# Optimization experiments

Measured on AMD Instinct MI355X. Metric: run time of the kernel, lower is better.

The kernel has to match this reference:

```python
import jax, jax.numpy as jnp
import numpy as np

B, T, F = 512, 256, 24
CF = 64            # cnn_filters
IN = 2 * CF        # LNN input size after second conv
UNITS = 128        # lnn_units
DENSE = 64         # dense_units
ODE_UNFOLDS = 6    # semi-implicit ODE solver unfolds (LiquidNet default)


def _maxpool1d(x):  # [B,C,T] -> [B,C,T//2]
    return jax.lax.reduce_window(x, -jnp.inf, jax.lax.max, (1, 1, 2), (1, 1, 2), 'VALID')


def setup_inputs() -> dict:
    key = jax.random.key(0)
    ks = jax.random.split(key, 16)
    u = lambda k, shape, lo, hi: jax.random.uniform(k, shape, jnp.float32, lo, hi)
    return {
        'x': jax.random.normal(ks[0], (B, T, F), jnp.float32),
        'conv1_w': jax.random.normal(ks[1], (CF, F, 5), jnp.float32) * 0.1,
        'conv1_b': jnp.zeros((CF,), jnp.float32),
        'conv2_w': jax.random.normal(ks[2], (2 * CF, CF, 3), jnp.float32) * 0.1,
        'conv2_b': jnp.zeros((2 * CF,), jnp.float32),
        'input_w': jnp.ones((IN,), jnp.float32),
        'input_b': jnp.zeros((IN,), jnp.float32),
        'sensory_mu': u(ks[3], (IN, UNITS), 0.3, 0.8),
        'sensory_sigma': u(ks[4], (IN, UNITS), 3.0, 8.0),
        'sensory_W': u(ks[5], (IN, UNITS), 0.01, 1.0),
        'sensory_erev': jnp.sign(jax.random.normal(ks[6], (IN, UNITS))).astype(jnp.float32),
        'mu': u(ks[7], (UNITS, UNITS), 0.3, 0.8),
        'sigma': u(ks[8], (UNITS, UNITS), 3.0, 8.0),
        'W': u(ks[9], (UNITS, UNITS), 0.01, 1.0),
        'erev': jnp.sign(jax.random.normal(ks[10], (UNITS, UNITS))).astype(jnp.float32),
        'vleak': u(ks[11], (UNITS,), -0.2, 0.2),
        'gleak': jnp.ones((UNITS,), jnp.float32),
        'cm_t': jnp.full((UNITS,), 0.5, jnp.float32),
        'fc1_w': jax.random.normal(ks[12], (DENSE, UNITS), jnp.float32) * 0.05,
        'fc1_b': jnp.zeros((DENSE,), jnp.float32),
        'fc2_w': jax.random.normal(ks[13], (1, DENSE), jnp.float32) * 0.05,
        'fc2_b': jnp.zeros((1,), jnp.float32),
    }


def _forward(x, conv1_w, conv1_b, conv2_w, conv2_b, input_w, input_b,
             sensory_mu, sensory_sigma, sensory_W, sensory_erev,
             mu, sigma, W, erev, vleak, gleak, cm_t,
             fc1_w, fc1_b, fc2_w, fc2_b):
    # --- CNN feature extractor ---
    h = jnp.transpose(x, (0, 2, 1))                        # [B, F, T]
    dn = ('NCH', 'OIH', 'NCH')
    h = jax.lax.conv_general_dilated(h, conv1_w, (1,), 'SAME', dimension_numbers=dn)
    h = _maxpool1d(jax.nn.relu(h + conv1_b[None, :, None]))
    h = jax.lax.conv_general_dilated(h, conv2_w, (1,), 'SAME', dimension_numbers=dn)
    h = _maxpool1d(jax.nn.relu(h + conv2_b[None, :, None]))  # dropout: eval mode (identity)
    feats = jnp.transpose(h, (0, 2, 1))                    # [B, T/4, IN]
    xs = jnp.transpose(feats, (1, 0, 2))                   # [T', B, IN] for scan

    # --- LiquidNet (LTC) recurrence, semi-implicit ODE solver ---
    def step(v, xt):
        xt = xt * input_w + input_b                        # affine input mapping
        s_act = sensory_W * jax.nn.sigmoid((xt[:, :, None] - sensory_mu) * sensory_sigma)  # [B,IN,U]
        w_num_s = jnp.sum(s_act * sensory_erev, axis=1)    # [B,U]
        w_den_s = jnp.sum(s_act, axis=1)
        for _ in range(ODE_UNFOLDS):
            w_act = W * jax.nn.sigmoid((v[:, :, None] - mu) * sigma)  # [B,U,U]
            w_num = jnp.sum(w_act * erev, axis=1) + w_num_s
            w_den = jnp.sum(w_act, axis=1) + w_den_s
            v = (cm_t * v + gleak * vleak + w_num) / (cm_t + gleak + w_den)
        return v, None

    h0 = jnp.zeros((x.shape[0], UNITS), x.dtype)
    hT, _ = jax.lax.scan(jax.checkpoint(step), h0, xs)

    # --- MLP head ---
    y = jax.nn.relu(hT @ fc1_w.T + fc1_b)
    return y @ fc2_w.T + fc2_b                             # [B, 1]


def reference(x, conv1_w, conv1_b, conv2_w, conv2_b, input_w, input_b,
              sensory_mu, sensory_sigma, sensory_W, sensory_erev,
              mu, sigma, W, erev, vleak, gleak, cm_t,
              fc1_w, fc1_b, fc2_w, fc2_b):
    return _forward(x, conv1_w, conv1_b, conv2_w, conv2_b, input_w, input_b,
                    sensory_mu, sensory_sigma, sensory_W, sensory_erev,
                    mu, sigma, W, erev, vleak, gleak, cm_t,
                    fc1_w, fc1_b, fc2_w, fc2_b)
```

## Files before the change

kernel.cpp:

```cpp
#include <hip/hip_runtime.h>
#include <hip/hip_bf16.h>


#define L2E 1.4426950408889634f

__global__ __launch_bounds__(256)
void prep_kernel(const float* __restrict__ smu, const float* __restrict__ ssig,
                 const float* __restrict__ sW,  const float* __restrict__ serev,
                 const float* __restrict__ mu,  const float* __restrict__ sig,
                 const float* __restrict__ W,   const float* __restrict__ erev,
                 const float* __restrict__ in_w, const float* __restrict__ in_b,
                 float2* __restrict__ R12, float* __restrict__ VT,
                 float4* __restrict__ S4) {
  int idx = blockIdx.x * 256 + threadIdx.x;
  int i = idx >> 7;
  float r1 = sig[idx] * L2E;
  R12[idx] = make_float2(r1, mu[idx] * r1);
  VT[idx]  = W[idx] * erev[idx];
  float ss = ssig[idx] * L2E;
  S4[idx] = make_float4(ss * in_w[i], (smu[idx] - in_b[i]) * ss,
                        sW[idx] * serev[idx], 0.f);
}

__launch_bounds__(512)
__global__ void conv1_kernel(const float* __restrict__ x, const float* __restrict__ w1,
                             const float* __restrict__ b1, float* __restrict__ P1) {
  __shared__ float xs[6240];
  int tid = threadIdx.x, b = blockIdx.x;
  const float* xb = x + (size_t)b * 6144;
  for (int idx = tid; idx < 6144; idx += 512) xs[idx + 48] = xb[idx];
  if (tid < 48) { xs[tid] = 0.f; xs[6192 + tid] = 0.f; }
  __syncthreads();
  int tp = tid & 127, cq = tid >> 7;
  float acc0[16], acc1[16];
#pragma unroll
  for (int n = 0; n < 16; n++) { float bb = b1[cq * 16 + n]; acc0[n] = bb; acc1[n] = bb; }
  for (int cic = 0; cic < 3; cic++) {
    float p[6][8];
#pragma unroll
    for (int r = 0; r < 6; r++) {
      const float* row = &xs[(2 * tp + r) * 24 + cic * 8];
      float4 a = *(const float4*)row;
      float4 c = *(const float4*)(row + 4);
      p[r][0] = a.x; p[r][1] = a.y; p[r][2] = a.z; p[r][3] = a.w;
      p[r][4] = c.x; p[r][5] = c.y; p[r][6] = c.z; p[r][7] = c.w;
    }
#pragma unroll
    for (int n = 0; n < 16; n++) {
      const float* wr = w1 + (cq * 16 + n) * 120 + cic * 40;
#pragma unroll
      for (int c = 0; c < 8; c++) {
#pragma unroll
        for (int kk = 0; kk < 5; kk++) {
          float w = wr[c * 5 + kk];
          acc0[n] = fmaf(p[kk][c],     w, acc0[n]);
          acc1[n] = fmaf(p[kk + 1][c], w, acc1[n]);
        }
      }
    }
  }
  float* pb = P1 + (size_t)b * 8192;
#pragma unroll
  for (int n = 0; n < 16; n++)
    pb[(cq * 16 + n) * 128 + tp] = fmaxf(fmaxf(acc0[n], acc1[n]), 0.f);
}

__launch_bounds__(512)
__global__ void conv2_kernel(const float* __restrict__ P1, const float* __restrict__ w2,
                             const float* __restrict__ b2, float* __restrict__ feats) {
  __shared__ float xs[8450];
  int tid = threadIdx.x, b = blockIdx.x;
  const float* pb = P1 + (size_t)b * 8192;
  for (int idx = tid; idx < 8192; idx += 512) {
    int ci = idx >> 7, t = idx & 127;
    xs[(t + 1) * 65 + ci] = pb[idx];
  }
  if (tid < 65) { xs[tid] = 0.f; xs[129 * 65 + tid] = 0.f; }
  __syncthreads();
  int tp = tid & 63, cq = tid >> 6;
  float acc0[16], acc1[16];
#pragma unroll
  for (int n = 0; n < 16; n++) { float bb = b2[cq * 16 + n]; acc0[n] = bb; acc1[n] = bb; }
  for (int cic = 0; cic < 8; cic++) {
    float p[4][8];
#pragma unroll
    for (int r = 0; r < 4; r++)
#pragma unroll
      for (int c = 0; c < 8; c++)
        p[r][c] = xs[(2 * tp + r) * 65 + cic * 8 + c];
#pragma unroll
    for (int n = 0; n < 16; n++) {
      const float* wr = w2 + (cq * 16 + n) * 192 + cic * 24;
#pragma unroll
      for (int c = 0; c < 8; c++) {
#pragma unroll
        for (int kk = 0; kk < 3; kk++) {
          float w = wr[c * 3 + kk];
          acc0[n] = fmaf(p[kk][c],     w, acc0[n]);
          acc1[n] = fmaf(p[kk + 1][c], w, acc1[n]);
        }
      }
    }
  }
  __syncthreads();
#pragma unroll
  for (int n = 0; n < 16; n += 4) {
    float4 v;
    v.x = fmaxf(fmaxf(acc0[n],     acc1[n]),     0.f);
    v.y = fmaxf(fmaxf(acc0[n + 1], acc1[n + 1]), 0.f);
    v.z = fmaxf(fmaxf(acc0[n + 2], acc1[n + 2]), 0.f);
    v.w = fmaxf(fmaxf(acc0[n + 3], acc1[n + 3]), 0.f);
    *(float4*)&xs[tp * 128 + cq * 16 + n] = v;
  }
  __syncthreads();
  float* fb = feats + (size_t)b * 8192;
  for (int idx = tid; idx < 8192; idx += 512) fb[idx] = xs[idx];
}

__launch_bounds__(1024)
__global__ void lnn_kernel(const float2* __restrict__ R12, const float* __restrict__ VT,
                           const float4* __restrict__ S4,
                           const float* __restrict__ feats,
                           const float* __restrict__ cm_t, const float* __restrict__ gleak,
                           const float* __restrict__ vleak,
                           const float* __restrict__ fc1_w, const float* __restrict__ fc1_b,
                           const float* __restrict__ fc2_w, const float* __restrict__ fc2_b,
                           float* __restrict__ out) {
  __shared__ float2 r12lds[16384];
  __shared__ float4 psum[8][128];
  __shared__ float2 vs2[128];
  __shared__ float2 xt2[128];
  __shared__ float red[2][64];
  int tid = threadIdx.x;
  int j = tid & 127, h = tid >> 7;
  int b0 = blockIdx.x * 2;

  for (int idx = tid; idx < 16384; idx += 1024) r12lds[idx] = R12[idx];

  float vw[16];
#pragma unroll
  for (int n = 0; n < 16; n++) vw[n] = VT[(16 * h + n) * 128 + j];

  float cmj = cm_t[j], glk = gleak[j];
  float gvl = glk * vleak[j], cgl = cmj + glk;
  float vj0 = 0.f, vj1 = 0.f;
  if (tid < 128) vs2[j] = make_float2(0.f, 0.f);
  __syncthreads();

  for (int t = 0; t < 64; t++) {
    if (tid < 128) {
      float a = feats[(size_t)b0 * 8192 + t * 128 + j];
      float b = feats[(size_t)(b0 + 1) * 8192 + t * 128 + j];
      xt2[j] = make_float2(a, b);
    }
    __syncthreads();

    float sn0 = 0.f, sd0 = 0.f, sn1 = 0.f, sd1 = 0.f;
    {
      float n0 = 0.f, d0 = 0.f, n1 = 0.f, d1 = 0.f;
      const float4* sp = S4 + (size_t)(16 * h) * 128 + j;
#pragma unroll 8
      for (int n = 0; n < 16; n++) {
        float4 s = sp[n * 128];
        float2 xv = xt2[16 * h + n];
        float q0 = __builtin_amdgcn_rcpf(1.f + __builtin_amdgcn_exp2f(fmaf(-s.x, xv.x, s.y)));
        n0 = fmaf(s.z, q0, n0); d0 = fmaf(fabsf(s.z), q0, d0);
        float q1 = __builtin_amdgcn_rcpf(1.f + __builtin_amdgcn_exp2f(fmaf(-s.x, xv.y, s.y)));
        n1 = fmaf(s.z, q1, n1); d1 = fmaf(fabsf(s.z), q1, d1);
      }
      psum[h][j] = make_float4(n0, d0, n1, d1);
    }
    __syncthreads();
    if (h == 0) {
      float4 a0 = psum[0][j], a1 = psum[1][j], a2 = psum[2][j], a3 = psum[3][j];
      float4 a4 = psum[4][j], a5 = psum[5][j], a6 = psum[6][j], a7 = psum[7][j];
      sn0 = a0.x + a1.x + a2.x + a3.x + a4.x + a5.x + a6.x + a7.x;
      sd0 = a0.y + a1.y + a2.y + a3.y + a4.y + a5.y + a6.y + a7.y;
      sn1 = a0.z + a1.z + a2.z + a3.z + a4.z + a5.z + a6.z + a7.z;
      sd1 = a0.w + a1.w + a2.w + a3.w + a4.w + a5.w + a6.w + a7.w;
    }
    __syncthreads();

    for (int u = 0; u < 6; u++) {
      float n0 = 0.f, d0 = 0.f, n1 = 0.f, d1 = 0.f;
      const float2* mp = &r12lds[(16 * h) * 128 + j];
#pragma unroll
      for (int n = 0; n < 16; n++) {
        float2 rr = mp[n * 128];
        float2 v2 = vs2[16 * h + n];
        float q0 = __builtin_amdgcn_rcpf(1.f + __builtin_amdgcn_exp2f(fmaf(-rr.x, v2.x, rr.y)));
        n0 = fmaf(vw[n], q0, n0); d0 = fmaf(fabsf(vw[n]), q0, d0);
        float q1 = __builtin_amdgcn_rcpf(1.f + __builtin_amdgcn_exp2f(fmaf(-rr.x, v2.y, rr.y)));
        n1 = fmaf(vw[n], q1, n1); d1 = fmaf(fabsf(vw[n]), q1, d1);
      }
      psum[h][j] = make_float4(n0, d0, n1, d1);
      __syncthreads();
      if (h == 0) {
        float4 a0 = psum[0][j], a1 = psum[1][j], a2 = psum[2][j], a3 = psum[3][j];
        float4 a4 = psum[4][j], a5 = psum[5][j], a6 = psum[6][j], a7 = psum[7][j];
        float wn0 = sn0 + a0.x + a1.x + a2.x + a3.x + a4.x + a5.x + a6.x + a7.x;
        float wd0 = sd0 + a0.y + a1.y + a2.y + a3.y + a4.y + a5.y + a6.y + a7.y;
        float wn1 = sn1 + a0.z + a1.z + a2.z + a3.z + a4.z + a5.z + a6.z + a7.z;
        float wd1 = sd1 + a0.w + a1.w + a2.w + a3.w + a4.w + a5.w + a6.w + a7.w;
        float den0 = cgl + wd0, den1 = cgl + wd1;
        float i0 = __builtin_amdgcn_rcpf(den0); i0 = i0 * fmaf(-den0, i0, 2.f);
        float i1 = __builtin_amdgcn_rcpf(den1); i1 = i1 * fmaf(-den1, i1, 2.f);
        vj0 = (fmaf(cmj, vj0, gvl) + wn0) * i0;
        vj1 = (fmaf(cmj, vj1, gvl) + wn1) * i1;
        vs2[j] = make_float2(vj0, vj1);
      }
      __syncthreads();
    }
  }

  if (tid < 128) {
    int g = tid >> 6, d = tid & 63;
    float acc = fc1_b[d];
    for (int u = 0; u < 128; u++) {
      float2 v2 = vs2[u];
      acc = fmaf(g ? v2.y : v2.x, fc1_w[d * 128 + u], acc);
    }
    red[g][d] = fmaxf(acc, 0.f) * fc2_w[d];
  }
  __syncthreads();
  if (tid < 2) {
    float s = fc2_b[0];
    for (int d = 0; d < 64; d++) s += red[tid][d];
    out[b0 + tid] = s;
  }
}

extern "C" void kernel_launch(void* const* d_in, const int* in_sizes, int n_in,
                              void* d_out, int out_size, void* d_ws, size_t ws_size,
                              hipStream_t stream) {
  (void)in_sizes; (void)n_in; (void)out_size; (void)ws_size;
  char* ws = (char*)d_ws;
  float*  P1   = (float*)(ws);
  float*  feats= (float*)(ws + (16 << 20));
  float2* R12  = (float2*)(ws + 0);
  float*  VT   = (float*)(ws + (128 << 10));
  float4* S4   = (float4*)(ws + (192 << 10));

  conv1_kernel<<<512, 512, 0, stream>>>((const float*)d_in[0],
      (const float*)d_in[1], (const float*)d_in[2], P1);
  conv2_kernel<<<512, 512, 0, stream>>>(P1,
      (const float*)d_in[3], (const float*)d_in[4], feats);
  prep_kernel<<<64, 256, 0, stream>>>(
      (const float*)d_in[7], (const float*)d_in[8],
      (const float*)d_in[9], (const float*)d_in[10],
      (const float*)d_in[11], (const float*)d_in[12],
      (const float*)d_in[13], (const float*)d_in[14],
      (const float*)d_in[5], (const float*)d_in[6],
      R12, VT, S4);
  lnn_kernel<<<256, 1024, 0, stream>>>(R12, VT, S4, feats,
      (const float*)d_in[17], (const float*)d_in[16], (const float*)d_in[15],
      (const float*)d_in[18], (const float*)d_in[19],
      (const float*)d_in[20], (const float*)d_in[21],
      (float*)d_out);
}
```

Before: 1.228 ms.

## Remap LNN threads so ODE reductions use wavefront shuffles and register-held weights

The LNN kernel's thread mapping changes so that the 8 partial-sum groups for each unit sit in adjacent lanes. Each ODE unfold can then reduce with xor shuffles, replacing the shared-memory psum exchange and one barrier per unfold. The recurrent weights R12 and VT move into registers, pre-transposed by the prep kernel, and all 64 timesteps of features are staged once into padded LDS. The sensory sum now seeds the recurrent accumulators, and the voltage buffer is double-buffered. The cost is higher register pressure at 1024 threads, and S4 global loads are now strided per timestep.

```diff
diff --git a/kernel.cpp b/kernel.cpp
--- a/kernel.cpp
+++ b/kernel.cpp
@@ -10,16 +10,18 @@
                  const float* __restrict__ mu,  const float* __restrict__ sig,
                  const float* __restrict__ W,   const float* __restrict__ erev,
                  const float* __restrict__ in_w, const float* __restrict__ in_b,
-                 float2* __restrict__ R12, float* __restrict__ VT,
-                 float4* __restrict__ S4) {
+                 float2* __restrict__ R12T, float* __restrict__ VTT,
+                 float4* __restrict__ S4T) {
   int idx = blockIdx.x * 256 + threadIdx.x;
-  int i = idx >> 7;
+  int i = idx >> 7, j = idx & 127;
+  int h = i >> 4, n = i & 15;
+  int dst = n * 1024 + j * 8 + h;
   float r1 = sig[idx] * L2E;
-  R12[idx] = make_float2(r1, mu[idx] * r1);
-  VT[idx]  = W[idx] * erev[idx];
+  R12T[dst] = make_float2(r1, mu[idx] * r1);
+  VTT[dst]  = W[idx] * erev[idx];
   float ss = ssig[idx] * L2E;
-  S4[idx] = make_float4(ss * in_w[i], (smu[idx] - in_b[i]) * ss,
-                        sW[idx] * serev[idx], 0.f);
+  S4T[dst] = make_float4(ss * in_w[i], (smu[idx] - in_b[i]) * ss,
+                         sW[idx] * serev[idx], 0.f);
 }
 
 __launch_bounds__(512)
@@ -118,96 +120,85 @@
 }
 
 __launch_bounds__(1024)
-__global__ void lnn_kernel(const float2* __restrict__ R12, const float* __restrict__ VT,
-                           const float4* __restrict__ S4,
+__global__ void lnn_kernel(const float2* __restrict__ R12T, const float* __restrict__ VTT,
+                           const float4* __restrict__ S4T,
                            const float* __restrict__ feats,
                            const float* __restrict__ cm_t, const float* __restrict__ gleak,
                            const float* __restrict__ vleak,
                            const float* __restrict__ fc1_w, const float* __restrict__ fc1_b,
                            const float* __restrict__ fc2_w, const float* __restrict__ fc2_b,
                            float* __restrict__ out) {
-  __shared__ float2 r12lds[16384];
-  __shared__ float4 psum[8][128];
-  __shared__ float2 vs2[128];
-  __shared__ float2 xt2[128];
+  __shared__ float2 xt_all[64][136];
+  __shared__ float2 vbuf[2][136];
   __shared__ float red[2][64];
   int tid = threadIdx.x;
-  int j = tid & 127, h = tid >> 7;
+  int h = tid & 7, j = tid >> 3;
   int b0 = blockIdx.x * 2;
 
-  for (int idx = tid; idx < 16384; idx += 1024) r12lds[idx] = R12[idx];
-
-  float vw[16];
-#pragma unroll
-  for (int n = 0; n < 16; n++) vw[n] = VT[(16 * h + n) * 128 + j];
+  {
+    const float* f0 = feats + (size_t)b0 * 8192;
+    const float* f1 = feats + (size_t)(b0 + 1) * 8192;
+    for (int idx = tid; idx < 8192; idx += 1024) {
+      int t = idx >> 7, u = idx & 127;
+      xt_all[t][u + (u >> 4)] = make_float2(f0[idx], f1[idx]);
+    }
+  }
+
+  float2 r12[16]; float vw[16];
+#pragma unroll
+  for (int n = 0; n < 16; n++) {
+    r12[n] = R12T[n * 1024 + tid];
+    vw[n]  = VTT[n * 1024 + tid];
+  }
 
   float cmj = cm_t[j], glk = gleak[j];
   float gvl = glk * vleak[j], cgl = cmj + glk;
   float vj0 = 0.f, vj1 = 0.f;
-  if (tid < 128) vs2[j] = make_float2(0.f, 0.f);
-  __syncthreads();
+  if (tid < 136) vbuf[0][tid] = make_float2(0.f, 0.f);
+  __syncthreads();
+
+  const float4* sp = S4T + tid;
+  const int hb = 17 * h;
 
   for (int t = 0; t < 64; t++) {
-    if (tid < 128) {
-      float a = feats[(size_t)b0 * 8192 + t * 128 + j];
-      float b = feats[(size_t)(b0 + 1) * 8192 + t * 128 + j];
-      xt2[j] = make_float2(a, b);
-    }
-    __syncthreads();
-
     float sn0 = 0.f, sd0 = 0.f, sn1 = 0.f, sd1 = 0.f;
-    {
-      float n0 = 0.f, d0 = 0.f, n1 = 0.f, d1 = 0.f;
-      const float4* sp = S4 + (size_t)(16 * h) * 128 + j;
 #pragma unroll 8
+    for (int n = 0; n < 16; n++) {
+      float4 s = sp[n * 1024];
+      float2 xv = xt_all[t][hb + n];
+      float q0 = __builtin_amdgcn_rcpf(1.f + __builtin_amdgcn_exp2f(fmaf(-s.x, xv.x, s.y)));
+      sn0 = fmaf(s.z, q0, sn0); sd0 = fmaf(fabsf(s.z), q0, sd0);
+      float q1 = __builtin_amdgcn_rcpf(1.f + __builtin_amdgcn_exp2f(fmaf(-s.x, xv.y, s.y)));
+      sn1 = fmaf(s.z, q1, sn1); sd1 = fmaf(fabsf(s.z), q1, sd1);
+    }
+
+#pragma unroll
+    for (int u = 0; u < 6; u++) {
+      float n0 = sn0, d0 = sd0, n1 = sn1, d1 = sd1;
+      const float2* vb = &vbuf[u & 1][hb];
+#pragma unroll
       for (int n = 0; n < 16; n++) {
-        float4 s = sp[n * 128];
-        float2 xv = xt2[16 * h + n];
-        float q0 = __builtin_amdgcn_rcpf(1.f + __builtin_amdgcn_exp2f(fmaf(-s.x, xv.x, s.y)));
-        n0 = fmaf(s.z, q0, n0); d0 = fmaf(fabsf(s.z), q0, d0);
-        float q1 = __builtin_amdgcn_rcpf(1.f + __builtin_amdgcn_exp2f(fmaf(-s.x, xv.y, s.y)));
-        n1 = fmaf(s.z, q1, n1); d1 = fmaf(fabsf(s.z), q1, d1);
-      }
-      psum[h][j] = make_float4(n0, d0, n1, d1);
-    }
-    __syncthreads();
-    if (h == 0) {
-      float4 a0 = psum[0][j], a1 = psum[1][j], a2 = psum[2][j], a3 = psum[3][j];
-      float4 a4 = psum[4][j], a5 = psum[5][j], a6 = psum[6][j], a7 = psum[7][j];
-      sn0 = a0.x + a1.x + a2.x + a3.x + a4.x + a5.x + a6.x + a7.x;
-      sd0 = a0.y + a1.y + a2.y + a3.y + a4.y + a5.y + a6.y + a7.y;
-      sn1 = a0.z + a1.z + a2.z + a3.z + a4.z + a5.z + a6.z + a7.z;
-      sd1 = a0.w + a1.w + a2.w + a3.w + a4.w + a5.w + a6.w + a7.w;
-    }
-    __syncthreads();
-
-    for (int u = 0; u < 6; u++) {
-      float n0 = 0.f, d0 = 0.f, n1 = 0.f, d1 = 0.f;
-      const float2* mp = &r12lds[(16 * h) * 128 + j];
-#pragma unroll
-      for (int n = 0; n < 16; n++) {
-        float2 rr = mp[n * 128];
-        float2 v2 = vs2[16 * h + n];
+        float2 rr = r12[n];
+        float2 v2 = vb[n];
         float q0 = __builtin_amdgcn_rcpf(1.f + __builtin_amdgcn_exp2f(fmaf(-rr.x, v2.x, rr.y)));
         n0 = fmaf(vw[n], q0, n0); d0 = fmaf(fabsf(vw[n]), q0, d0);
         float q1 = __builtin_amdgcn_rcpf(1.f + __builtin_amdgcn_exp2f(fmaf(-rr.x, v2.y, rr.y)));
         n1 = fmaf(vw[n], q1, n1); d1 = fmaf(fabsf(vw[n]), q1, d1);
       }
-      psum[h][j] = make_float4(n0, d0, n1, d1);
-      __syncthreads();
+#pragma unroll
+      for (int m = 1; m < 8; m <<= 1) {
+        n0 += __shfl_xor(n0, m, 64);
+        d0 += __shfl_xor(d0, m, 64);
+        n1 += __shfl_xor(n1, m, 64);
+        d1 += __shfl_xor(d1, m, 64);
+      }
       if (h == 0) {
-        float4 a0 = psum[0][j], a1 = psum[1][j], a2 = psum[2][j], a3 = psum[3][j];
-        float4 a4 = psum[4][j], a5 = psum[5][j], a6 = psum[6][j], a7 = psum[7][j];
-        float wn0 = sn0 + a0.x + a1.x + a2.x + a3.x + a4.x + a5.x + a6.x + a7.x;
-        float wd0 = sd0 + a0.y + a1.y + a2.y + a3.y + a4.y + a5.y + a6.y + a7.y;
-        float wn1 = sn1 + a0.z + a1.z + a2.z + a3.z + a4.z + a5.z + a6.z + a7.z;
-        float wd1 = sd1 + a0.w + a1.w + a2.w + a3.w + a4.w + a5.w + a6.w + a7.w;
-        float den0 = cgl + wd0, den1 = cgl + wd1;
+        float den0 = cgl + d0, den1 = cgl + d1;
         float i0 = __builtin_amdgcn_rcpf(den0); i0 = i0 * fmaf(-den0, i0, 2.f);
         float i1 = __builtin_amdgcn_rcpf(den1); i1 = i1 * fmaf(-den1, i1, 2.f);
-        vj0 = (fmaf(cmj, vj0, gvl) + wn0) * i0;
-        vj1 = (fmaf(cmj, vj1, gvl) + wn1) * i1;
-        vs2[j] = make_float2(vj0, vj1);
+        vj0 = (fmaf(cmj, vj0, gvl) + n0) * i0;
+        vj1 = (fmaf(cmj, vj1, gvl) + n1) * i1;
+        vbuf[(u + 1) & 1][j + (j >> 4)] = make_float2(vj0, vj1);
       }
       __syncthreads();
     }
@@ -217,7 +208,7 @@
     int g = tid >> 6, d = tid & 63;
     float acc = fc1_b[d];
     for (int u = 0; u < 128; u++) {
-      float2 v2 = vs2[u];
+      float2 v2 = vbuf[0][u + (u >> 4)];
       acc = fmaf(g ? v2.y : v2.x, fc1_w[d * 128 + u], acc);
     }
     red[g][d] = fmaxf(acc, 0.f) * fc2_w[d];
@@ -237,9 +228,9 @@
   char* ws = (char*)d_ws;
   float*  P1   = (float*)(ws);
   float*  feats= (float*)(ws + (16 << 20));
-  float2* R12  = (float2*)(ws + 0);
-  float*  VT   = (float*)(ws + (128 << 10));
-  float4* S4   = (float4*)(ws + (192 << 10));
+  float2* R12T = (float2*)(ws + 0);
+  float*  VTT  = (float*)(ws + (128 << 10));
+  float4* S4T  = (float4*)(ws + (192 << 10));
 
   conv1_kernel<<<512, 512, 0, stream>>>((const float*)d_in[0],
       (const float*)d_in[1], (const float*)d_in[2], P1);
@@ -251,8 +242,8 @@
       (const float*)d_in[11], (const float*)d_in[12],
       (const float*)d_in[13], (const float*)d_in[14],
       (const float*)d_in[5], (const float*)d_in[6],
-      R12, VT, S4);
-  lnn_kernel<<<256, 1024, 0, stream>>>(R12, VT, S4, feats,
+      R12T, VTT, S4T);
+  lnn_kernel<<<256, 1024, 0, stream>>>(R12T, VTT, S4T, feats,
       (const float*)d_in[17], (const float*)d_in[16], (const float*)d_in[15],
       (const float*)d_in[18], (const float*)d_in[19],
       (const float*)d_in[20], (const float*)d_in[21],
```

After: 2.005 ms. 63.2% more time.
